# Kernel optimization log

Measured on AMD Instinct MI355X. Metric: run time of the kernel, lower is better.

## Reference

```python
import jax, jax.numpy as jnp
import numpy as np

B, S, HID = 2, 2048, 2048
H, KV, D = 32, 4, 128
G = H // KV
EPS = 1e-6
SCALE = D ** -0.5
ROPE_THETA = 1000000.0


def setup_inputs() -> dict:
    key = jax.random.key(0)
    ks = jax.random.split(key, 6)
    hidden_states = jax.random.normal(ks[0], (B, S, HID), jnp.float32)
    # real RoPE tables (position_embeddings passed into forward)
    inv_freq = 1.0 / (ROPE_THETA ** (np.arange(0, D, 2, dtype=np.float32) / D))
    ang = np.arange(S, dtype=np.float32)[:, None] * inv_freq[None, :]  # [S, D/2]
    emb = np.concatenate([ang, ang], axis=-1)  # [S, D]
    cos = jnp.broadcast_to(jnp.asarray(np.cos(emb)), (B, S, D))
    sin = jnp.broadcast_to(jnp.asarray(np.sin(emb)), (B, S, D))
    sd = 0.02
    wq = jax.random.normal(ks[1], (H * D, HID), jnp.float32) * sd
    wk = jax.random.normal(ks[2], (KV * D, HID), jnp.float32) * sd
    wv = jax.random.normal(ks[3], (KV * D, HID), jnp.float32) * sd
    wo = jax.random.normal(ks[4], (HID, H * D), jnp.float32) * sd
    q_norm_w = jnp.ones((D,), jnp.float32)
    k_norm_w = jnp.ones((D,), jnp.float32)
    return {"hidden_states": hidden_states, "cos": cos, "sin": sin,
            "wq": wq, "wk": wk, "wv": wv, "wo": wo,
            "q_norm_w": q_norm_w, "k_norm_w": k_norm_w}


def _rms_norm(x, w):
    var = jnp.mean(jnp.square(x), axis=-1, keepdims=True)
    return x * jax.lax.rsqrt(var + EPS) * w


def _rotate_half(x):
    x1, x2 = jnp.split(x, 2, axis=-1)
    return jnp.concatenate([-x2, x1], axis=-1)


def _rope(x, cos, sin):
    # x: [B,S,N,D]; cos/sin: [B,S,1,D] (unsqueeze_dim=2)
    return x * cos + _rotate_half(x) * sin


def reference(hidden_states, cos, sin, wq, wk, wv, wo, q_norm_w, k_norm_w):
    x = hidden_states
    q = jnp.einsum('bsh,oh->bso', x, wq).reshape(B, S, H, D)
    k = jnp.einsum('bsh,oh->bso', x, wk).reshape(B, S, KV, D)
    v = jnp.einsum('bsh,oh->bso', x, wv).reshape(B, S, KV, D)
    q = _rms_norm(q, q_norm_w)
    k = _rms_norm(k, k_norm_w)
    c = cos[:, :, None, :]
    s = sin[:, :, None, :]
    q = _rope(q, c, s)
    k = _rope(k, c, s)
    # GQA causal attention, BSND layout
    qg = q.reshape(B, S, KV, G, D)
    scores = jnp.einsum('bqkgd,bskd->bkgqs', qg, k) * SCALE  # [B,KV,G,Sq,Sk]
    causal = jnp.tril(jnp.ones((S, S), bool))
    scores = jnp.where(causal, scores, jnp.finfo(scores.dtype).min)
    p = jax.nn.softmax(scores, axis=-1)
    out = jnp.einsum('bkgqs,bskd->bqkgd', p, v).reshape(B, S, H * D)
    return jnp.einsum('bso,ho->bsh', out, wo)
```

## Files before the change

kernel.cpp:

```cpp
#include <hip/hip_runtime.h>
#include <hip/hip_bf16.h>

typedef __attribute__((ext_vector_type(8))) short short8;
typedef __attribute__((ext_vector_type(4))) float f32x4;

#define DEVI static __device__ __forceinline__

constexpr int Bb = 2, Ss = 2048, Hh = 32, KVc = 4, Dc = 128;
constexpr float EPSc = 1e-6f;
constexpr float SCALEc = 0.08838834764831845f;

DEVI float bf2f(short s) {
  unsigned u = ((unsigned)(unsigned short)s) << 16;
  float f; __builtin_memcpy(&f, &u, 4); return f;
}
DEVI short f2bf(float f) {
  __hip_bfloat16 h = __float2bfloat16(f);
  unsigned short u; __builtin_memcpy(&u, &h, 2); return (short)u;
}

#define GLDS(gsrc, ldst) __builtin_amdgcn_global_load_lds( \
    (const __attribute__((address_space(1))) void*)(gsrc), \
    (__attribute__((address_space(3))) void*)(ldst), 16, 0, 0)

struct Cvt5 { const float* src[5]; short* dst[5]; };
__global__ void cvt_all(Cvt5 a) {
  constexpr int CUM[6] = {0, 2097152, 4194304, 4456448, 4718592, 6815744};
  const int stride = gridDim.x * blockDim.x;
  for (int i = blockIdx.x * blockDim.x + threadIdx.x; i < 6815744; i += stride) {
    int s = 0;
#pragma unroll
    for (int t = 1; t < 5; ++t) if (i >= CUM[t]) s = t;
    int j = i - CUM[s];
    float4 v = ((const float4*)a.src[s])[j];
    short4 o;
    o.x = f2bf(v.x); o.y = f2bf(v.y); o.z = f2bf(v.z); o.w = f2bf(v.w);
    ((short4*)a.dst[s])[j] = o;
  }
}

__launch_bounds__(512, 2)
__global__ void gemm8q(const short* __restrict__ A,
                       const short* __restrict__ Bp,
                       short* __restrict__ oq,
                       const float* __restrict__ cosb,
                       const float* __restrict__ sinb,
                       const float* __restrict__ qnw,
                       int K)
{
  __shared__ short lA[2][256 * 64];
  __shared__ short lB[2][256 * 64];

  const int tid = threadIdx.x, lane = tid & 63;
  const int wvi = tid >> 6;
  const int l15 = lane & 15, g = lane >> 4;
  const int wm = wvi >> 1, wn = wvi & 1;
  const int m0 = blockIdx.x * 256;
  const int n0 = blockIdx.y * 256;

  f32x4 acc[4][8] = {};

  auto stA = [&](int half, int slot, int kt) {
#pragma unroll
    for (int j = 0; j < 2; ++j) {
      int rr = j * 64 + (tid >> 3);
      int grow = ((rr >> 5) << 6) + half * 32 + (rr & 31);
      GLDS(A + (size_t)(m0 + grow) * K + kt * 64 + (((tid & 7) ^ (rr & 7)) << 3),
           &lA[slot][(half * 128 + j * 64) * 64 + tid * 8]);
    }
  };
  auto stB = [&](int half, int slot, int kt) {
#pragma unroll
    for (int j = 0; j < 2; ++j) {
      int rr = j * 64 + (tid >> 3);
      int gn = ((rr >> 6) << 7) + half * 64 + (rr & 63);
      GLDS(Bp + (size_t)(n0 + gn) * K + kt * 64 + (((tid & 7) ^ (rr & 7)) << 3),
           &lB[slot][(half * 128 + j * 64) * 64 + tid * 8]);
    }
  };

#define PH(SLOT, MH, NH, STG, GT) do {                                          \
    short8 afr[2][2], bfr[4][2];                                                \
    _Pragma("unroll")                                                           \
    for (int mi2 = 0; mi2 < 2; ++mi2) {                                         \
      int rp = (MH) * 128 + wm * 32 + mi2 * 16 + l15;                           \
      _Pragma("unroll")                                                         \
      for (int kk = 0; kk < 2; ++kk)                                            \
        afr[mi2][kk] = *(const short8*)(&lA[SLOT][rp * 64 +                     \
                         (((kk * 4 + g) ^ (rp & 7)) << 3)]);                    \
    }                                                                           \
    _Pragma("unroll")                                                           \
    for (int nj = 0; nj < 4; ++nj) {                                            \
      int rp = (NH) * 128 + wn * 64 + nj * 16 + l15;                            \
      _Pragma("unroll")                                                         \
      for (int kk = 0; kk < 2; ++kk)                                            \
        bfr[nj][kk] = *(const short8*)(&lB[SLOT][rp * 64 +                      \
                         (((kk * 4 + g) ^ (rp & 7)) << 3)]);                    \
    }                                                                           \
    STG;                                                                        \
    asm volatile("" ::: "memory");                                              \
    __builtin_amdgcn_s_barrier();                                               \
    __builtin_amdgcn_s_setprio(1);                                              \
    _Pragma("unroll")                                                           \
    for (int mi2 = 0; mi2 < 2; ++mi2)                                           \
      _Pragma("unroll")                                                         \
      for (int nj = 0; nj < 4; ++nj)                                            \
        _Pragma("unroll")                                                       \
        for (int kk = 0; kk < 2; ++kk)                                          \
          acc[(MH)*2 + mi2][(NH)*4 + nj] =                                      \
            __builtin_amdgcn_mfma_f32_16x16x32_bf16(afr[mi2][kk], bfr[nj][kk],  \
                acc[(MH)*2 + mi2][(NH)*4 + nj], 0, 0, 0);                       \
    __builtin_amdgcn_s_setprio(0);                                              \
    GT;                                                                         \
    asm volatile("" ::: "memory");                                              \
    __builtin_amdgcn_s_barrier();                                               \
  } while (0)

  const int nit = K >> 7;

  stA(0, 0, 0); stB(0, 0, 0); stA(1, 0, 0); stB(1, 0, 0);
  stA(0, 1, 1); stB(0, 1, 1);
  asm volatile("s_waitcnt vmcnt(4)" ::: "memory");
  __builtin_amdgcn_s_barrier();

  for (int it = 0; it < nit; ++it) {
    const int kt1 = 2 * it + 1;
    const int k2 = 2 * it + 2, k3 = 2 * it + 3;
    const bool pre = (it + 1 < nit);
    PH(0, 0, 0, { stA(1, 1, kt1); }, {});
    PH(0, 0, 1, { stB(1, 1, kt1); }, {});
    PH(0, 1, 0, { if (pre) stA(0, 0, k2); }, {});
    PH(0, 1, 1, { if (pre) stB(0, 0, k2); },
               { if (pre) asm volatile("s_waitcnt vmcnt(4)" ::: "memory");
                 else     asm volatile("s_waitcnt vmcnt(0)" ::: "memory"); });
    PH(1, 0, 0, { if (pre) stA(1, 0, k2); }, {});
    PH(1, 0, 1, { if (pre) stB(1, 0, k2); }, {});
    PH(1, 1, 0, { if (pre) stA(0, 1, k3); }, {});
    PH(1, 1, 1, { if (pre) stB(0, 1, k3); },
               { if (pre) asm volatile("s_waitcnt vmcnt(4)" ::: "memory"); });
  }
#undef PH

  float w8[8];
#pragma unroll
  for (int ni = 0; ni < 8; ++ni) w8[ni] = qnw[ni * 16 + l15];
#pragma unroll
  for (int mi = 0; mi < 4; ++mi)
#pragma unroll
    for (int r = 0; r < 4; ++r) {
      int m = m0 + wm * 64 + mi * 16 + g * 4 + r;
      int b = m >> 11, s = m & 2047;
      float xv[8];
      float ssq = 0.f;
#pragma unroll
      for (int ni = 0; ni < 8; ++ni) { xv[ni] = acc[mi][ni][r]; ssq += xv[ni] * xv[ni]; }
      ssq += __shfl_xor(ssq, 1);
      ssq += __shfl_xor(ssq, 2);
      ssq += __shfl_xor(ssq, 4);
      ssq += __shfl_xor(ssq, 8);
      float inv = rsqrtf(ssq * (1.0f / 128.0f) + EPSc);
      float xn[8];
#pragma unroll
      for (int ni = 0; ni < 8; ++ni) xn[ni] = xv[ni] * inv * w8[ni];
      const float* cpr = cosb + ((size_t)b * Ss + s) * Dc;
      const float* spr = sinb + ((size_t)b * Ss + s) * Dc;
#pragma unroll
      for (int ni = 0; ni < 8; ++ni) {
        int d = ni * 16 + l15;
        float c = cpr[d], sn = spr[d];
        float rot = (ni < 4) ? -xn[ni + 4] : xn[ni - 4];
        float o = xn[ni] * c + rot * sn;
        oq[(size_t)m * 4096 + n0 + wn * 128 + d] = f2bf(o * SCALEc);
      }
    }
}

template<int MODE>
__launch_bounds__(256, 4)
__global__ void gemm2(const short* __restrict__ A,
                      const short* __restrict__ B1,
                      const short* __restrict__ B2,
                      short* __restrict__ ok,
                      short* __restrict__ ov,
                      float* __restrict__ of,
                      const float* __restrict__ cosb,
                      const float* __restrict__ sinb,
                      const float* __restrict__ knw,
                      int K)
{
  __shared__ short lA[2][128 * 32];
  __shared__ short lB[2][128 * 32];
  const int tid = threadIdx.x;
  const int lane = tid & 63;
  const int wvi = tid >> 6;
  const int l15 = lane & 15, g = lane >> 4;
  const int m0 = blockIdx.x * 128;
  const int nt = blockIdx.y;
  const short* Bp; int n0, region;
  if (MODE == 0) {
    if (nt < 4) { Bp = B1; n0 = nt * 128;       region = 1; }
    else        { Bp = B2; n0 = (nt - 4) * 128; region = 2; }
  } else { Bp = B1; n0 = nt * 128; region = 3; }

  const int wrow = wvi * 32;
  const int srow = tid >> 2, schunk = tid & 3;

  f32x4 acc[2][8] = {};

  auto STAGE = [&](int ks, int bufi) {
    const int k0 = ks * 32;
#pragma unroll
    for (int c = 0; c < 2; ++c) {
      int row = c * 64 + srow;
      int gc = schunk ^ ((row >> 1) & 3);
      GLDS(A  + (size_t)(m0 + row) * K + k0 + gc * 8, &lA[bufi][(c * 256 + tid) * 8]);
      GLDS(Bp + (size_t)(n0 + row) * K + k0 + gc * 8, &lB[bufi][(c * 256 + tid) * 8]);
    }
  };

  const int nks = K >> 5;
  STAGE(0, 0);
  STAGE(1, 1);

  for (int ks = 0; ks < nks; ++ks) {
    const int cb = ks & 1;
    if (ks + 1 < nks) asm volatile("s_waitcnt vmcnt(4)" ::: "memory");
    else              asm volatile("s_waitcnt vmcnt(0)" ::: "memory");
    __builtin_amdgcn_s_barrier();
    asm volatile("" ::: "memory");

    short8 afr[2], bfr[8];
#pragma unroll
    for (int i = 0; i < 2; ++i) {
      int ra = wrow + i * 16 + l15;
      afr[i] = *(const short8*)(&lA[cb][0] + ra * 32 + ((g ^ ((ra >> 1) & 3)) * 8));
    }
#pragma unroll
    for (int i = 0; i < 8; ++i) {
      int rb = i * 16 + l15;
      bfr[i] = *(const short8*)(&lB[cb][0] + rb * 32 + ((g ^ ((rb >> 1) & 3)) * 8));
    }
#pragma unroll
    for (int mi = 0; mi < 2; ++mi)
#pragma unroll
      for (int ni = 0; ni < 8; ++ni)
        acc[mi][ni] = __builtin_amdgcn_mfma_f32_16x16x32_bf16(afr[mi], bfr[ni], acc[mi][ni], 0, 0, 0);

    asm volatile("" ::: "memory");
    __builtin_amdgcn_s_barrier();
    if (ks + 2 < nks) STAGE(ks + 2, cb);
  }

  if (MODE == 1) {
#pragma unroll
    for (int mi = 0; mi < 2; ++mi)
#pragma unroll
      for (int r = 0; r < 4; ++r) {
        int m = m0 + wrow + mi * 16 + g * 4 + r;
#pragma unroll
        for (int ni = 0; ni < 8; ++ni)
          of[(size_t)m * 2048 + n0 + ni * 16 + l15] = acc[mi][ni][r];
      }
  } else if (region == 2) {
#pragma unroll
    for (int mi = 0; mi < 2; ++mi)
#pragma unroll
      for (int r = 0; r < 4; ++r) {
        int m = m0 + wrow + mi * 16 + g * 4 + r;
        int b = m >> 11, s = m & 2047;
#pragma unroll
        for (int ni = 0; ni < 8; ++ni) {
          int n = n0 + ni * 16 + l15;
          int kvi = n >> 7, d = n & 127;
          ov[(((size_t)b * KVc + kvi) * 128 + d) * Ss + s] = f2bf(acc[mi][ni][r]);
        }
      }
  } else {
    float w8[8];
#pragma unroll
    for (int ni = 0; ni < 8; ++ni) w8[ni] = knw[ni * 16 + l15];
#pragma unroll
    for (int mi = 0; mi < 2; ++mi)
#pragma unroll
      for (int r = 0; r < 4; ++r) {
        int m = m0 + wrow + mi * 16 + g * 4 + r;
        int b = m >> 11, s = m & 2047;
        float xv[8];
        float ssq = 0.f;
#pragma unroll
        for (int ni = 0; ni < 8; ++ni) { xv[ni] = acc[mi][ni][r]; ssq += xv[ni] * xv[ni]; }
        ssq += __shfl_xor(ssq, 1);
        ssq += __shfl_xor(ssq, 2);
        ssq += __shfl_xor(ssq, 4);
        ssq += __shfl_xor(ssq, 8);
        float inv = rsqrtf(ssq * (1.0f / 128.0f) + EPSc);
        float xn[8];
#pragma unroll
        for (int ni = 0; ni < 8; ++ni) xn[ni] = xv[ni] * inv * w8[ni];
        const float* cpr = cosb + ((size_t)b * Ss + s) * Dc;
        const float* spr = sinb + ((size_t)b * Ss + s) * Dc;
#pragma unroll
        for (int ni = 0; ni < 8; ++ni) {
          int dl = ni * 16 + l15;
          float c = cpr[dl], sn = spr[dl];
          float rot = (ni < 4) ? -xn[ni + 4] : xn[ni - 4];
          float o = xn[ni] * c + rot * sn;
          int n = n0 + dl;
          int kvi = n >> 7, d = n & 127;
          ok[(((size_t)b * KVc + kvi) * Ss + s) * 128 + d] = f2bf(o);
        }
      }
  }
}

__launch_bounds__(256, 2)
__global__ void attn_fwd(const short* __restrict__ qb,
                         const short* __restrict__ kbuf,
                         const short* __restrict__ vtbuf,
                         short* __restrict__ ob)
{
  __shared__ short lK[2][64 * 128];
  __shared__ short lV[2][128 * 64];
  __shared__ short lP[4][32 * 32];
  const int tid = threadIdx.x, lane = tid & 63, wvi = tid >> 6;
  const int l15 = lane & 15, g = lane >> 4;
  const int pi = blockIdx.x, h = blockIdx.y, b = blockIdx.z;
  const int kv = h >> 3;
  const short* kp = kbuf  + ((size_t)b * KVc + kv) * Ss * 128;
  const short* vp = vtbuf + ((size_t)b * KVc + kv) * 128 * Ss;
  const int krow = tid >> 4, kch = tid & 15;
  const int vrow = tid >> 3, vch = tid & 7;

  for (int which = 0; which < 2; ++which) {
    const int qt = which ? (15 - pi) : pi;
    const int qwb = qt * 128 + wvi * 32;
    const int nkt = 2 * qt + 2;

    short8 qf[2][4];
#pragma unroll
    for (int qs = 0; qs < 2; ++qs)
#pragma unroll
      for (int dc = 0; dc < 4; ++dc)
        qf[qs][dc] = *(const short8*)(qb + (size_t)(b * Ss + qwb + qs * 16 + l15) * 4096
                                         + h * 128 + dc * 32 + g * 8);

    f32x4 oacc[2][8] = {};
    float mrun[2] = { -__builtin_inff(), -__builtin_inff() };
    float lrun[2] = { 0.f, 0.f };

    auto STAGE = [&](int kt, int bufi) {
      const int kb0 = kt * 64;
#pragma unroll
      for (int c = 0; c < 4; ++c) {
        int r = c * 16 + krow;
        int gc = kch ^ (r & 7);
        GLDS(kp + (size_t)(kb0 + r) * 128 + gc * 8, &lK[bufi][(c * 256 + tid) * 8]);
      }
#pragma unroll
      for (int c = 0; c < 4; ++c) {
        int r = c * 32 + vrow;
        int gc = vch ^ (r & 7);
        GLDS(vp + (size_t)r * Ss + kb0 + gc * 8, &lV[bufi][(c * 256 + tid) * 8]);
      }
    };

    STAGE(0, 0);
    STAGE(1, 1);

    for (int kt = 0; kt < nkt; ++kt) {
      const int cb = kt & 1;
      if (kt + 1 < nkt) asm volatile("s_waitcnt vmcnt(8)" ::: "memory");
      else              asm volatile("s_waitcnt vmcnt(0)" ::: "memory");
      __builtin_amdgcn_s_barrier();
      asm volatile("" ::: "memory");

#pragma unroll
      for (int half = 0; half < 2; ++half) {
        const int kb0 = kt * 64 + half * 32;
        if (kb0 <= qwb + 31) {
          short8 kf[2][4];
#pragma unroll
          for (int ks = 0; ks < 2; ++ks)
#pragma unroll
            for (int dc = 0; dc < 4; ++dc) {
              int row = half * 32 + ks * 16 + l15;
              kf[ks][dc] = *(const short8*)(&lK[cb][0] + row * 128 + (((dc * 4 + g) ^ (row & 7)) * 8));
            }
          f32x4 st[2][2] = {};
          __builtin_amdgcn_s_setprio(1);
#pragma unroll
          for (int qs = 0; qs < 2; ++qs)
#pragma unroll
            for (int ks = 0; ks < 2; ++ks)
#pragma unroll
              for (int dc = 0; dc < 4; ++dc)
                st[qs][ks] = __builtin_amdgcn_mfma_f32_16x16x32_bf16(kf[ks][dc], qf[qs][dc], st[qs][ks], 0, 0, 0);
          __builtin_amdgcn_s_setprio(0);

          const bool need_mask = (kb0 + 31 > qwb);
#pragma unroll
          for (int qs = 0; qs < 2; ++qs) {
            const int qg = qwb + qs * 16 + l15;
            float p[8];
            float tmax = -__builtin_inff();
#pragma unroll
            for (int ks = 0; ks < 2; ++ks)
#pragma unroll
              for (int r = 0; r < 4; ++r) {
                float v = st[qs][ks][r];
                if (need_mask && (kb0 + ks * 16 + g * 4 + r > qg)) v = -__builtin_inff();
                p[ks * 4 + r] = v;
                tmax = fmaxf(tmax, v);
              }
            tmax = fmaxf(tmax, __shfl_xor(tmax, 16));
            tmax = fmaxf(tmax, __shfl_xor(tmax, 32));
            float m_use = mrun[qs];
            if (__any(tmax > m_use + 8.0f)) {
              float mnew = fmaxf(m_use, tmax);
              float scl = __expf(m_use - mnew);
              lrun[qs] *= scl;
              mrun[qs] = mnew;
#pragma unroll
              for (int r = 0; r < 4; ++r) {
                float sc = __shfl(scl, g * 4 + r);
#pragma unroll
                for (int dt = 0; dt < 8; ++dt)
                  oacc[qs][dt][r] *= sc;
              }
              m_use = mnew;
            }
            float rsum = 0.f;
#pragma unroll
            for (int j = 0; j < 8; ++j) { p[j] = __expf(p[j] - m_use); rsum += p[j]; }
            rsum += __shfl_xor(rsum, 16);
            rsum += __shfl_xor(rsum, 32);
            lrun[qs] += rsum;
            {
              int row = qs * 16 + l15;
              int sw = (row >> 1) & 3;
              short* pr = lP[wvi] + row * 32;
#pragma unroll
              for (int ks = 0; ks < 2; ++ks) {
                int idx = (((2 * ks + (g >> 1)) ^ sw) * 8) + (g & 1) * 4;
                short4 pw;
                pw.x = f2bf(p[ks * 4 + 0]);
                pw.y = f2bf(p[ks * 4 + 1]);
                pw.z = f2bf(p[ks * 4 + 2]);
                pw.w = f2bf(p[ks * 4 + 3]);
                *(short4*)(pr + idx) = pw;
              }
            }
          }
          asm volatile("" ::: "memory");
          short8 vf[8];
#pragma unroll
          for (int dt = 0; dt < 8; ++dt) {
            int row = dt * 16 + l15;
            vf[dt] = *(const short8*)(&lV[cb][0] + row * 64 + (((half * 4 + g) ^ (row & 7)) * 8));
          }
          __builtin_amdgcn_s_setprio(1);
#pragma unroll
          for (int qs = 0; qs < 2; ++qs) {
            int row = qs * 16 + l15;
            short8 pf = *(const short8*)(lP[wvi] + row * 32 + ((g ^ ((row >> 1) & 3)) * 8));
#pragma unroll
            for (int dt = 0; dt < 8; ++dt)
              oacc[qs][dt] = __builtin_amdgcn_mfma_f32_16x16x32_bf16(pf, vf[dt], oacc[qs][dt], 0, 0, 0);
          }
          __builtin_amdgcn_s_setprio(0);
          asm volatile("" ::: "memory");
        }
      }

      asm volatile("" ::: "memory");
      __builtin_amdgcn_s_barrier();
      if (kt + 2 < nkt) STAGE(kt + 2, cb);
    }

#pragma unroll
    for (int qs = 0; qs < 2; ++qs)
#pragma unroll
      for (int r = 0; r < 4; ++r) {
        float inv = 1.0f / __shfl(lrun[qs], g * 4 + r);
        int qrow = qwb + qs * 16 + g * 4 + r;
        short* op = ob + (size_t)(b * Ss + qrow) * 4096 + h * 128;
#pragma unroll
        for (int dt = 0; dt < 8; ++dt)
          op[dt * 16 + l15] = f2bf(oacc[qs][dt][r] * inv);
      }
  }
}

extern "C" void kernel_launch(void* const* d_in, const int* in_sizes, int n_in,
                              void* d_out, int out_size, void* d_ws, size_t ws_size,
                              hipStream_t stream) {
  const float* x    = (const float*)d_in[0];
  const float* cosb = (const float*)d_in[1];
  const float* sinb = (const float*)d_in[2];
  const float* wq   = (const float*)d_in[3];
  const float* wk   = (const float*)d_in[4];
  const float* wv   = (const float*)d_in[5];
  const float* wo   = (const float*)d_in[6];
  const float* qw   = (const float*)d_in[7];
  const float* kw   = (const float*)d_in[8];

  size_t off = 0;
  auto alloc = [&](size_t bytes) {
    char* p = (char*)d_ws + off;
    off += (bytes + 255) & ~(size_t)255;
    return p;
  };
  short* x_bf  = (short*)alloc((size_t)8388608 * 2);
  short* wq_bf = (short*)alloc((size_t)8388608 * 2);
  short* wk_bf = (short*)alloc((size_t)1048576 * 2);
  short* wv_bf = (short*)alloc((size_t)1048576 * 2);
  short* wo_bf = (short*)alloc((size_t)8388608 * 2);
  short* q_bf  = (short*)alloc((size_t)16777216 * 2);
  short* k_bf  = (short*)alloc((size_t)2097152 * 2);
  short* v_bf  = (short*)alloc((size_t)2097152 * 2);
  short* ao_bf = (short*)alloc((size_t)16777216 * 2);

  Cvt5 ca;
  ca.src[0] = x;    ca.dst[0] = x_bf;
  ca.src[1] = wq;   ca.dst[1] = wq_bf;
  ca.src[2] = wk;   ca.dst[2] = wk_bf;
  ca.src[3] = wv;   ca.dst[3] = wv_bf;
  ca.src[4] = wo;   ca.dst[4] = wo_bf;
  cvt_all<<<2048, 256, 0, stream>>>(ca);

  gemm8q<<<dim3(16, 16), 512, 0, stream>>>(x_bf, wq_bf, q_bf, cosb, sinb, qw, 2048);
  gemm2<0><<<dim3(32, 8), 256, 0, stream>>>(x_bf, wk_bf, wv_bf, k_bf, v_bf, nullptr,
                                            cosb, sinb, kw, 2048);
  attn_fwd<<<dim3(8, 32, 2), 256, 0, stream>>>(q_bf, k_bf, v_bf, ao_bf);
  gemm2<1><<<dim3(32, 16), 256, 0, stream>>>(ao_bf, wo_bf, nullptr, nullptr, nullptr,
                                             (float*)d_out, nullptr, nullptr, nullptr, 4096);
}
```

Baseline: 346.4 us.

## Use split-K 256x256 GEMM for output projection and exp2 softmax

The output projection moves from the smaller gemm2 tile to the 256x256 gemm8 kernel with a two-way split over K. Each half writes an fp32 partial, and a separate add kernel sums them. The softmax now uses exp2 with log2(e) folded into the Q scaling, and the rescale threshold is widened to match. The attention wave-to-query mapping is also changed to (wvi&3). The split-K path adds an extra fp32 buffer, more output traffic and an extra launch in exchange for larger tiles and more parallelism.

After: 380.3 us. 9.8% more time.

```diff
diff --git a/kernel.cpp b/kernel.cpp
--- a/kernel.cpp
+++ b/kernel.cpp
@@ -9,6 +9,8 @@
 constexpr int Bb = 2, Ss = 2048, Hh = 32, KVc = 4, Dc = 128;
 constexpr float EPSc = 1e-6f;
 constexpr float SCALEc = 0.08838834764831845f;
+constexpr float LOG2Ec = 1.4426950408889634f;
+constexpr float SCALE2c = SCALEc * LOG2Ec;
 
 DEVI float bf2f(short s) {
   unsigned u = ((unsigned)(unsigned short)s) << 16;
@@ -39,14 +41,27 @@
   }
 }
 
+__global__ void add_part(float* __restrict__ out, const float* __restrict__ part, int n4) {
+  int i = blockIdx.x * blockDim.x + threadIdx.x;
+  if (i < n4) {
+    float4 o = ((const float4*)out)[i];
+    float4 p = ((const float4*)part)[i];
+    o.x += p.x; o.y += p.y; o.z += p.z; o.w += p.w;
+    ((float4*)out)[i] = o;
+  }
+}
+
+template<int MODE>
 __launch_bounds__(512, 2)
-__global__ void gemm8q(const short* __restrict__ A,
-                       const short* __restrict__ Bp,
-                       short* __restrict__ oq,
-                       const float* __restrict__ cosb,
-                       const float* __restrict__ sinb,
-                       const float* __restrict__ qnw,
-                       int K)
+__global__ void gemm8(const short* __restrict__ A,
+                      const short* __restrict__ Bp,
+                      short* __restrict__ oq,
+                      float* __restrict__ of0,
+                      float* __restrict__ of1,
+                      const float* __restrict__ cosb,
+                      const float* __restrict__ sinb,
+                      const float* __restrict__ qnw,
+                      int Kstride)
 {
   __shared__ short lA[2][256 * 64];
   __shared__ short lB[2][256 * 64];
@@ -57,6 +72,7 @@
   const int wm = wvi >> 1, wn = wvi & 1;
   const int m0 = blockIdx.x * 256;
   const int n0 = blockIdx.y * 256;
+  const int koff = (MODE == 1) ? (int)blockIdx.z * 2048 : 0;
 
   f32x4 acc[4][8] = {};
 
@@ -65,7 +81,7 @@
     for (int j = 0; j < 2; ++j) {
       int rr = j * 64 + (tid >> 3);
       int grow = ((rr >> 5) << 6) + half * 32 + (rr & 31);
-      GLDS(A + (size_t)(m0 + grow) * K + kt * 64 + (((tid & 7) ^ (rr & 7)) << 3),
+      GLDS(A + (size_t)(m0 + grow) * Kstride + koff + kt * 64 + (((tid & 7) ^ (rr & 7)) << 3),
            &lA[slot][(half * 128 + j * 64) * 64 + tid * 8]);
     }
   };
@@ -74,7 +90,7 @@
     for (int j = 0; j < 2; ++j) {
       int rr = j * 64 + (tid >> 3);
       int gn = ((rr >> 6) << 7) + half * 64 + (rr & 63);
-      GLDS(Bp + (size_t)(n0 + gn) * K + kt * 64 + (((tid & 7) ^ (rr & 7)) << 3),
+      GLDS(Bp + (size_t)(n0 + gn) * Kstride + koff + kt * 64 + (((tid & 7) ^ (rr & 7)) << 3),
            &lB[slot][(half * 128 + j * 64) * 64 + tid * 8]);
     }
   };
@@ -116,7 +132,7 @@
     __builtin_amdgcn_s_barrier();                                               \
   } while (0)
 
-  const int nit = K >> 7;
+  const int nit = 2048 >> 7;
 
   stA(0, 0, 0); stB(0, 0, 0); stA(1, 0, 0); stB(1, 0, 0);
   stA(0, 1, 1); stB(0, 1, 1);
@@ -141,38 +157,51 @@
   }
 #undef PH
 
-  float w8[8];
-#pragma unroll
-  for (int ni = 0; ni < 8; ++ni) w8[ni] = qnw[ni * 16 + l15];
-#pragma unroll
-  for (int mi = 0; mi < 4; ++mi)
-#pragma unroll
-    for (int r = 0; r < 4; ++r) {
-      int m = m0 + wm * 64 + mi * 16 + g * 4 + r;
-      int b = m >> 11, s = m & 2047;
-      float xv[8];
-      float ssq = 0.f;
-#pragma unroll
-      for (int ni = 0; ni < 8; ++ni) { xv[ni] = acc[mi][ni][r]; ssq += xv[ni] * xv[ni]; }
-      ssq += __shfl_xor(ssq, 1);
-      ssq += __shfl_xor(ssq, 2);
-      ssq += __shfl_xor(ssq, 4);
-      ssq += __shfl_xor(ssq, 8);
-      float inv = rsqrtf(ssq * (1.0f / 128.0f) + EPSc);
-      float xn[8];
-#pragma unroll
-      for (int ni = 0; ni < 8; ++ni) xn[ni] = xv[ni] * inv * w8[ni];
-      const float* cpr = cosb + ((size_t)b * Ss + s) * Dc;
-      const float* spr = sinb + ((size_t)b * Ss + s) * Dc;
-#pragma unroll
-      for (int ni = 0; ni < 8; ++ni) {
-        int d = ni * 16 + l15;
-        float c = cpr[d], sn = spr[d];
-        float rot = (ni < 4) ? -xn[ni + 4] : xn[ni - 4];
-        float o = xn[ni] * c + rot * sn;
-        oq[(size_t)m * 4096 + n0 + wn * 128 + d] = f2bf(o * SCALEc);
-      }
-    }
+  if (MODE == 1) {
+    float* of = blockIdx.z ? of1 : of0;
+#pragma unroll
+    for (int mi = 0; mi < 4; ++mi)
+#pragma unroll
+      for (int r = 0; r < 4; ++r) {
+        int m = m0 + wm * 64 + mi * 16 + g * 4 + r;
+#pragma unroll
+        for (int ni = 0; ni < 8; ++ni)
+          of[(size_t)m * 2048 + n0 + wn * 128 + ni * 16 + l15] = acc[mi][ni][r];
+      }
+  } else {
+    float w8[8];
+#pragma unroll
+    for (int ni = 0; ni < 8; ++ni) w8[ni] = qnw[ni * 16 + l15];
+#pragma unroll
+    for (int mi = 0; mi < 4; ++mi)
+#pragma unroll
+      for (int r = 0; r < 4; ++r) {
+        int m = m0 + wm * 64 + mi * 16 + g * 4 + r;
+        int b = m >> 11, s = m & 2047;
+        float xv[8];
+        float ssq = 0.f;
+#pragma unroll
+        for (int ni = 0; ni < 8; ++ni) { xv[ni] = acc[mi][ni][r]; ssq += xv[ni] * xv[ni]; }
+        ssq += __shfl_xor(ssq, 1);
+        ssq += __shfl_xor(ssq, 2);
+        ssq += __shfl_xor(ssq, 4);
+        ssq += __shfl_xor(ssq, 8);
+        float inv = rsqrtf(ssq * (1.0f / 128.0f) + EPSc);
+        float xn[8];
+#pragma unroll
+        for (int ni = 0; ni < 8; ++ni) xn[ni] = xv[ni] * inv * w8[ni];
+        const float* cpr = cosb + ((size_t)b * Ss + s) * Dc;
+        const float* spr = sinb + ((size_t)b * Ss + s) * Dc;
+#pragma unroll
+        for (int ni = 0; ni < 8; ++ni) {
+          int d = ni * 16 + l15;
+          float c = cpr[d], sn = spr[d];
+          float rot = (ni < 4) ? -xn[ni + 4] : xn[ni - 4];
+          float o = xn[ni] * c + rot * sn;
+          oq[(size_t)m * 4096 + n0 + wn * 128 + d] = f2bf(o * SCALE2c);
+        }
+      }
+  }
 }
 
 template<int MODE>
@@ -333,7 +362,7 @@
 
   for (int which = 0; which < 2; ++which) {
     const int qt = which ? (15 - pi) : pi;
-    const int qwb = qt * 128 + wvi * 32;
+    const int qwb = qt * 128 + (wvi & 3) * 32;
     const int nkt = 2 * qt + 2;
 
     short8 qf[2][4];
@@ -415,9 +444,9 @@
             tmax = fmaxf(tmax, __shfl_xor(tmax, 16));
             tmax = fmaxf(tmax, __shfl_xor(tmax, 32));
             float m_use = mrun[qs];
-            if (__any(tmax > m_use + 8.0f)) {
+            if (__any(tmax > m_use + 11.0f)) {
               float mnew = fmaxf(m_use, tmax);
-              float scl = __expf(m_use - mnew);
+              float scl = exp2f(m_use - mnew);
               lrun[qs] *= scl;
               mrun[qs] = mnew;
 #pragma unroll
@@ -431,7 +460,7 @@
             }
             float rsum = 0.f;
 #pragma unroll
-            for (int j = 0; j < 8; ++j) { p[j] = __expf(p[j] - m_use); rsum += p[j]; }
+            for (int j = 0; j < 8; ++j) { p[j] = exp2f(p[j] - m_use); rsum += p[j]; }
             rsum += __shfl_xor(rsum, 16);
             rsum += __shfl_xor(rsum, 32);
             lrun[qs] += rsum;
@@ -519,6 +548,8 @@
   short* k_bf  = (short*)alloc((size_t)2097152 * 2);
   short* v_bf  = (short*)alloc((size_t)2097152 * 2);
   short* ao_bf = (short*)alloc((size_t)16777216 * 2);
+  float* part1 = (float*)alloc((size_t)8388608 * 4);
+  const bool splitk_ok = (off <= ws_size);
 
   Cvt5 ca;
   ca.src[0] = x;    ca.dst[0] = x_bf;
@@ -528,10 +559,17 @@
   ca.src[4] = wo;   ca.dst[4] = wo_bf;
   cvt_all<<<2048, 256, 0, stream>>>(ca);
 
-  gemm8q<<<dim3(16, 16), 512, 0, stream>>>(x_bf, wq_bf, q_bf, cosb, sinb, qw, 2048);
+  gemm8<0><<<dim3(16, 16), 512, 0, stream>>>(x_bf, wq_bf, q_bf, nullptr, nullptr,
+                                             cosb, sinb, qw, 2048);
   gemm2<0><<<dim3(32, 8), 256, 0, stream>>>(x_bf, wk_bf, wv_bf, k_bf, v_bf, nullptr,
                                             cosb, sinb, kw, 2048);
   attn_fwd<<<dim3(8, 32, 2), 256, 0, stream>>>(q_bf, k_bf, v_bf, ao_bf);
-  gemm2<1><<<dim3(32, 16), 256, 0, stream>>>(ao_bf, wo_bf, nullptr, nullptr, nullptr,
-                                             (float*)d_out, nullptr, nullptr, nullptr, 4096);
-}
+  if (splitk_ok) {
+    gemm8<1><<<dim3(16, 8, 2), 512, 0, stream>>>(ao_bf, wo_bf, nullptr, (float*)d_out, part1,
+                                                 nullptr, nullptr, nullptr, 4096);
+    add_part<<<8192, 256, 0, stream>>>((float*)d_out, part1, 2097152);
+  } else {
+    gemm2<1><<<dim3(32, 16), 256, 0, stream>>>(ao_bf, wo_bf, nullptr, nullptr, nullptr,
+                                               (float*)d_out, nullptr, nullptr, nullptr, 4096);
+  }
+}
```
